# Optimization experiments

Measured on AMD Instinct MI355X. Metric: run time of the kernel, lower is better.

Reference implementation:

```python
import jax, jax.numpy as jnp
import numpy as np

LEVELS = ((64, 176), (32, 88), (16, 44), (8, 22))
S_TOTAL = sum(h * w for h, w in LEVELS)  # 14960
C = 128; HH = 8; HD = 16; R = 4; L = 4; P = 8
G = 32; PC_MIN = -4.0; PC_MAX = 4.0
NUM_CLASSES = 17; PROP = 3 + 3 + 4 + 1 + NUM_CLASSES  # 28


def _ln(x, g, b):
    m = x.mean(-1, keepdims=True)
    v = ((x - m) ** 2).mean(-1, keepdims=True)
    return (x - m) * jax.lax.rsqrt(v + 1e-5) * g + b


def setup_inputs() -> dict:
    key = jax.random.key(0)
    ks = jax.random.split(key, 20)
    B, N, CAM = 1, 1024, 6
    d = {}
    d['query'] = jax.random.normal(ks[0], (B, N, C), jnp.float32)
    d['gaussian_props'] = jax.random.normal(ks[1], (B, N, PROP), jnp.float32)
    d['ms_feats'] = jax.random.normal(ks[2], (B, CAM, S_TOTAL, C), jnp.float32)
    d['depth_maps'] = jax.random.uniform(ks[3], (B, CAM, 64, 176), jnp.float32, 0.5, 50.0)
    d['lidar2img'] = jax.random.normal(ks[4], (B, CAM, 4, 4), jnp.float32)
    d['img_h'] = 256
    d['img_w'] = 704
    w = lambda k, shp: jax.random.normal(k, shp, jnp.float32) * 0.02
    d['W_sc'] = w(ks[5], (3, 3, 3, C, C)); d['b_sc'] = jnp.zeros((C,), jnp.float32)
    d['sc_g'] = jnp.ones((C,), jnp.float32); d['sc_b'] = jnp.zeros((C,), jnp.float32)
    d['ref_off_w'] = w(ks[6], (C, R * 3)); d['ref_off_b'] = jnp.zeros((R * 3,), jnp.float32)
    d['off_w'] = w(ks[7], (C, HH * R * L * P * 2)); d['off_b'] = jnp.zeros((HH * R * L * P * 2,), jnp.float32)
    d['aw_w'] = w(ks[8], (C, HH * R * L * P)); d['aw_b'] = jnp.zeros((HH * R * L * P,), jnp.float32)
    d['val_w'] = w(ks[9], (C, C)); d['val_b'] = jnp.zeros((C,), jnp.float32)
    d['out_w'] = w(ks[10], (C, C)); d['out_b'] = jnp.zeros((C,), jnp.float32)
    d['an_g'] = jnp.ones((C,), jnp.float32); d['an_b'] = jnp.zeros((C,), jnp.float32)
    d['f1_w'] = w(ks[11], (C, 4 * C)); d['f1_b'] = jnp.zeros((4 * C,), jnp.float32)
    d['f2_w'] = w(ks[12], (4 * C, C)); d['f2_b'] = jnp.zeros((C,), jnp.float32)
    d['fn_g'] = jnp.ones((C,), jnp.float32); d['fn_b'] = jnp.zeros((C,), jnp.float32)
    d['p1_w'] = w(ks[13], (C, C)); d['p1_b'] = jnp.zeros((C,), jnp.float32)
    d['p2_w'] = w(ks[14], (C, PROP)); d['p2_b'] = jnp.zeros((PROP,), jnp.float32)
    return d


def _forward(query, gaussian_props, ms_feats, depth_maps, lidar2img,
             W_sc, b_sc, sc_g, sc_b, ref_off_w, ref_off_b, off_w, off_b,
             aw_w, aw_b, val_w, val_b, out_w, out_b, an_g, an_b,
             f1_w, f1_b, f2_w, f2_b, fn_g, fn_b, p1_w, p1_b, p2_w, p2_b,
             img_h, img_w):
    B, N, _ = query.shape
    CAM = ms_feats.shape[1]
    means = gaussian_props[..., :3]
    # ---- SparseConv3DBlock: scatter-mean voxelization, 3x3x3 conv, gather back ----
    vs = (PC_MAX - PC_MIN) / G
    vox = jnp.clip(jnp.floor((means - PC_MIN) / vs).astype(jnp.int32), 0, G - 1)
    flat = (vox[..., 0] * G + vox[..., 1]) * G + vox[..., 2]  # [B,N]
    bi = jnp.arange(B)[:, None]
    grid = jnp.zeros((B, G * G * G, C), query.dtype).at[bi, flat].add(query)
    cnt = jnp.zeros((B, G * G * G, 1), query.dtype).at[bi, flat].add(1.0)
    grid = (grid / jnp.maximum(cnt, 1.0)).reshape(B, G, G, G, C)
    grid = jax.lax.conv_general_dilated(grid, W_sc, (1, 1, 1), 'SAME',
                                        dimension_numbers=('NDHWC', 'DHWIO', 'NDHWC')) + b_sc
    grid = jax.nn.gelu(grid).reshape(B, G * G * G, C)
    query = _ln(query + grid[bi, flat], sc_g, sc_b)
    # ---- DeformableAttention3D ----
    fW = jnp.asarray(img_w, query.dtype); fH = jnp.asarray(img_h, query.dtype)
    ref3d = means[:, :, None, :] + (query @ ref_off_w + ref_off_b).reshape(B, N, R, 3)
    pts = jnp.concatenate([ref3d, jnp.ones_like(ref3d[..., :1])], -1)
    proj = jnp.einsum('bcij,bnrj->bcnri', lidar2img, pts)  # [B,CAM,N,R,4]
    z = proj[..., 2]; zc = jnp.maximum(z, 1e-5)
    u = proj[..., 0] / zc; v = proj[..., 1] / zc
    valid = (z > 1e-5) & (u >= 0) & (u < fW) & (v >= 0) & (v < fH)
    Hd, Wd = depth_maps.shape[2], depth_maps.shape[3]
    iu = jnp.clip((u / fW * Wd).astype(jnp.int32), 0, Wd - 1)
    iv = jnp.clip((v / fH * Hd).astype(jnp.int32), 0, Hd - 1)
    ds = jnp.take_along_axis(depth_maps.reshape(B, CAM, Hd * Wd),
                             (iv * Wd + iu).reshape(B, CAM, N * R), axis=2).reshape(B, CAM, N, R)
    wmask = jnp.exp(-jnp.abs(z - ds)) * valid.astype(query.dtype)  # [B,CAM,N,R]
    ref2 = jnp.stack([u / fW, v / fH], -1)  # [B,CAM,N,R,2]
    offs = (query @ off_w + off_b).reshape(B, N, HH, R, L, P, 2)
    attn = jax.nn.softmax((query @ aw_w + aw_b).reshape(B, N, HH, R * L * P), -1)
    attn = attn.reshape(B, N, HH, R, L, P)
    value = (ms_feats @ val_w + val_b).reshape(B, CAM, S_TOTAL, HH, HD)
    out = jnp.zeros((B, N, HH, HD), query.dtype)
    s0 = 0
    for l, (Hl, Wl) in enumerate(LEVELS):
        sz = Hl * Wl
        vl = value[:, :, s0:s0 + sz].transpose(0, 1, 3, 2, 4).reshape(B * CAM, HH, sz, HD)
        s0 += sz
        off_l = offs[:, :, :, :, l]  # [B,N,HH,R,P,2]
        loc = ref2[:, :, :, None, :, None, :] + off_l[:, None] / jnp.array([Wl, Hl], query.dtype)
        # loc: [B,CAM,N,HH,R,P,2] in normalized coords
        x = (loc[..., 0] * Wl - 0.5).transpose(0, 1, 3, 2, 4, 5).reshape(B * CAM, HH, N * R * P)
        y = (loc[..., 1] * Hl - 0.5).transpose(0, 1, 3, 2, 4, 5).reshape(B * CAM, HH, N * R * P)
        x0 = jnp.floor(x); y0 = jnp.floor(y); wx = x - x0; wy = y - y0
        x0i = jnp.clip(x0.astype(jnp.int32), 0, Wl - 1)
        x1i = jnp.clip(x0.astype(jnp.int32) + 1, 0, Wl - 1)
        y0i = jnp.clip(y0.astype(jnp.int32), 0, Hl - 1)
        y1i = jnp.clip(y0.astype(jnp.int32) + 1, 0, Hl - 1)
        g = lambda ix, iy: jnp.take_along_axis(vl, (iy * Wl + ix)[..., None], axis=2)
        samp = (((1 - wx) * (1 - wy))[..., None] * g(x0i, y0i)
                + (wx * (1 - wy))[..., None] * g(x1i, y0i)
                + ((1 - wx) * wy)[..., None] * g(x0i, y1i)
                + (wx * wy)[..., None] * g(x1i, y1i))  # [B*CAM,HH,N*R*P,HD]
        samp = samp.reshape(B, CAM, HH, N, R, P, HD)
        ws = attn[:, :, :, :, l, :][:, None].transpose(0, 1, 3, 2, 4, 5) * wmask[:, :, None, :, :, None]
        out = out + jnp.einsum('bchnrp,bchnrpd->bnhd', ws, samp)
    attn_out = out.reshape(B, N, C) @ out_w + out_b
    query = _ln(query + attn_out, an_g, an_b)
    query = _ln(query + (jax.nn.gelu(query @ f1_w + f1_b) @ f2_w + f2_b), fn_g, fn_b)
    props = gaussian_props + (jax.nn.gelu(query @ p1_w + p1_b) @ p2_w + p2_b)
    return query, props


def reference(query, gaussian_props, ms_feats, depth_maps, lidar2img,
              W_sc, b_sc, sc_g, sc_b, ref_off_w, ref_off_b, off_w, off_b,
              aw_w, aw_b, val_w, val_b, out_w, out_b, an_g, an_b,
              f1_w, f1_b, f2_w, f2_b, fn_g, fn_b, p1_w, p1_b, p2_w, p2_b,
              img_h, img_w):
    return _forward(query, gaussian_props, ms_feats, depth_maps, lidar2img,
                    W_sc, b_sc, sc_g, sc_b, ref_off_w, ref_off_b, off_w, off_b,
                    aw_w, aw_b, val_w, val_b, out_w, out_b, an_g, an_b,
                    f1_w, f1_b, f2_w, f2_b, fn_g, fn_b, p1_w, p1_b, p2_w, p2_b,
                    img_h, img_w)
```

## Files before the change

### kernel.cpp

```cpp
#include <hip/hip_runtime.h>
#include <hip/hip_bf16.h>
#include <math.h>

#define NQ    1024
#define CC    128
#define CAM   6
#define RR    4
#define LL    4
#define PP    8
#define HHD   8
#define HDD   16
#define GG    32
#define S_TOT 14960
#define PROPN 28
#define NTAP  27
#define MVAL  (CAM * S_TOT)
#define NVB   ((MVAL + 63) / 64)
#define NCVB  (8 * NTAP)

typedef __attribute__((ext_vector_type(8))) short bf16x8;
typedef __attribute__((ext_vector_type(4))) float f32x4;

__device__ __forceinline__ float gelu_tanh(float x) {
    return 0.5f * x * (1.0f + tanhf(0.7978845608028654f * (x + 0.044715f * x * x * x)));
}

__device__ __forceinline__ unsigned short f2bf(float f) {
    union { float f; unsigned int u; } x; x.f = f;
    unsigned int r = (x.u + 0x7FFFu + ((x.u >> 16) & 1u)) >> 16;
    return (unsigned short)r;
}

__device__ __forceinline__ float bf2f(short s) {
    union { unsigned int u; float f; } x;
    x.u = ((unsigned int)(unsigned short)s) << 16;
    return x.f;
}

__global__ void k_wt_scatter(const float* __restrict__ Wsc, unsigned short* __restrict__ WscT,
                             const float* __restrict__ valw, unsigned short* __restrict__ valwT,
                             const float* __restrict__ outw, unsigned short* __restrict__ outwT,
                             const float* __restrict__ p1w, unsigned short* __restrict__ p1wT,
                             const float* __restrict__ f1w, unsigned short* __restrict__ f1wT,
                             const float* __restrict__ f2w, unsigned short* __restrict__ f2wT,
                             const float* __restrict__ offw, unsigned short* __restrict__ offwT,
                             const float* __restrict__ aww, unsigned short* __restrict__ awwT,
                             const float* __restrict__ p2w, unsigned short* __restrict__ p2wT,
                             const float* __restrict__ p2b, float* __restrict__ p2bp,
                             const float* __restrict__ qin, const float* __restrict__ gp,
                             float* __restrict__ grid, float* __restrict__ cnt,
                             int* __restrict__ flatidx) {
    __shared__ float t[64][65];
    __shared__ int sflat[2];
    int z = blockIdx.z;
    int tid = threadIdx.x;

    if (z >= 63) {
        int half = tid >> 7, c = tid & 127;
        int n = ((z - 63) * 4 + (blockIdx.x * 2 + blockIdx.y)) * 2 + half;
        if (c == 0) {
            float mx = gp[n * PROPN + 0], my = gp[n * PROPN + 1], mz = gp[n * PROPN + 2];
            int vx = (int)floorf((mx + 4.0f) * 4.0f);
            int vy = (int)floorf((my + 4.0f) * 4.0f);
            int vz = (int)floorf((mz + 4.0f) * 4.0f);
            vx = min(max(vx, 0), GG - 1);
            vy = min(max(vy, 0), GG - 1);
            vz = min(max(vz, 0), GG - 1);
            int f = (vx * GG + vy) * GG + vz;
            sflat[half] = f;
            flatidx[n] = f;
            atomicAdd(&cnt[f], 1.0f);
        }
        __syncthreads();
        atomicAdd(&grid[(size_t)sflat[half] * CC + c], qin[(size_t)n * CC + c]);
        return;
    }

    int n0 = blockIdx.x * 64, k0 = blockIdx.y * 64;
    if (z == 62) {
#pragma unroll
        for (int it = 0; it < 16; ++it) {
            int idx = tid + it * 256;
            int r = idx >> 6, c = idx & 63;
            t[r][c] = (n0 + c < PROPN) ? p2w[(size_t)(k0 + r) * PROPN + n0 + c] : 0.f;
        }
        __syncthreads();
#pragma unroll
        for (int it = 0; it < 16; ++it) {
            int idx = tid + it * 256;
            int r = idx >> 6, c = idx & 63;
            p2wT[(size_t)(n0 + r) * 128 + k0 + c] = f2bf(t[c][r]);
        }
        if (blockIdx.x == 0 && blockIdx.y == 0 && tid < 128)
            p2bp[tid] = (tid < PROPN) ? p2b[tid] : 0.f;
        return;
    }
    const float* src; unsigned short* dst; int ss, ds;
    if (z < 27)       { src = Wsc + (size_t)z * 16384; dst = WscT + (size_t)z * 16384; ss = 128; ds = 128; }
    else if (z == 27) { src = valw; dst = valwT; ss = 128; ds = 128; }
    else if (z == 28) { src = outw; dst = outwT; ss = 128; ds = 128; }
    else if (z == 29) { src = p1w;  dst = p1wT;  ss = 128; ds = 128; }
    else if (z < 34)  { int q = z - 30; src = f1w + q * 128; dst = f1wT + (size_t)q * 16384; ss = 512;  ds = 128; }
    else if (z < 38)  { int q = z - 34; src = f2w + (size_t)q * 16384; dst = f2wT + q * 128; ss = 128;  ds = 512; }
    else if (z < 54)  { int q = z - 38; src = offw + q * 128; dst = offwT + (size_t)q * 16384; ss = 2048; ds = 128; }
    else              { int q = z - 54; src = aww + q * 128;  dst = awwT + (size_t)q * 16384; ss = 1024; ds = 128; }
#pragma unroll
    for (int it = 0; it < 16; ++it) {
        int idx = tid + it * 256;
        int r = idx >> 6, c = idx & 63;
        t[r][c] = src[(size_t)(k0 + r) * ss + n0 + c];
    }
    __syncthreads();
#pragma unroll
    for (int it = 0; it < 16; ++it) {
        int idx = tid + it * 256;
        int r = idx >> 6, c = idx & 63;
        dst[(size_t)(n0 + r) * ds + k0 + c] = f2bf(t[c][r]);
    }
}

union CVSm {
    struct { bf16x8 As[128 * 16]; bf16x8 Bs[128 * 16]; } c;
    struct { bf16x8 Bs[128 * 16]; unsigned short Os[64 * 128]; float sbias[128]; } v;
};
__global__ __launch_bounds__(256) void k_conv_val(
    const float* __restrict__ grid, const float* __restrict__ cnt,
    const int* __restrict__ flatidx, const unsigned short* __restrict__ WT,
    float* __restrict__ convacc27,
    const float* __restrict__ ms, const unsigned short* __restrict__ valwT,
    const float* __restrict__ valb, unsigned short* __restrict__ value)
{
    __shared__ CVSm sm;
    __shared__ int   nbase[128];
    __shared__ float nscale[128];
    int bx = blockIdx.x, tid = threadIdx.x;
    int lane = tid & 63, wv = tid >> 6;
    int r = lane & 15, q = lane >> 4;

    if (bx >= NCVB) {
        int vb = bx - NCVB;
        int m0 = vb * 64;
#pragma unroll
        for (int it = 0; it < 8; ++it) {
            int idx = tid + it * 256;
            int n = idx >> 4, c = idx & 15;
            sm.v.Bs[n * 16 + (c ^ (n & 15))] = *(const bf16x8*)(valwT + (size_t)n * 128 + c * 8);
        }
        if (tid < 128) sm.v.sbias[tid] = valb[tid];
        __syncthreads();

        int row = m0 + wv * 16 + r;
        int mg = min(row, MVAL - 1);
        const float* pA = ms + (size_t)mg * 128;

        f32x4 acc[8];
#pragma unroll
        for (int j = 0; j < 8; ++j)
#pragma unroll
            for (int e = 0; e < 4; ++e) acc[j][e] = 0.f;

#pragma unroll
        for (int ks = 0; ks < 4; ++ks) {
            const float* p = pA + ks * 32 + q * 8;
            float4 aa = *(const float4*)p;
            float4 bb = *(const float4*)(p + 4);
            bf16x8 af;
            af[0] = (short)f2bf(aa.x); af[1] = (short)f2bf(aa.y);
            af[2] = (short)f2bf(aa.z); af[3] = (short)f2bf(aa.w);
            af[4] = (short)f2bf(bb.x); af[5] = (short)f2bf(bb.y);
            af[6] = (short)f2bf(bb.z); af[7] = (short)f2bf(bb.w);
            bf16x8 bfr[8];
#pragma unroll
            for (int j = 0; j < 8; ++j)
                bfr[j] = sm.v.Bs[(j * 16 + r) * 16 + ((ks * 4 + q) ^ r)];
#pragma unroll
            for (int j = 0; j < 8; ++j)
                acc[j] = __builtin_amdgcn_mfma_f32_16x16x32_bf16(af, bfr[j], acc[j], 0, 0, 0);
        }

#pragma unroll
        for (int j = 0; j < 8; ++j)
#pragma unroll
            for (int e = 0; e < 4; ++e) {
                int rl = wv * 16 + q * 4 + e;
                sm.v.Os[rl * 128 + j * 16 + r] = f2bf(acc[j][e] + sm.v.sbias[j * 16 + r]);
            }
        __syncthreads();
#pragma unroll
        for (int it = 0; it < 2; ++it) {
            int idx = tid + it * 256;
            int rl = idx & 63, h = idx >> 6;
            int m = m0 + rl;
            if (m < MVAL) {
                int cam = m / S_TOT;
                int s = m - cam * S_TOT;
                int pos, HW, sb;
                if (s < 11264)      { pos = s;          HW = 11264; sb = 0; }
                else if (s < 14080) { pos = s - 11264;  HW = 2816;  sb = 11264; }
                else if (s < 14784) { pos = s - 14080;  HW = 704;   sb = 14080; }
                else                { pos = s - 14784;  HW = 176;   sb = 14784; }
                size_t dst = ((size_t)cam * S_TOT + sb) * CC
                           + (size_t)h * (HW * HDD) + (size_t)pos * HDD;
                *(bf16x8*)(value + dst)     = *(const bf16x8*)&sm.v.Os[rl * 128 + h * 16];
                *(bf16x8*)(value + dst + 8) = *(const bf16x8*)&sm.v.Os[rl * 128 + h * 16 + 8];
            }
        }
        return;
    }

    int tap = bx >> 3;
    int q0 = (bx & 7) * 128;
    int dz = tap / 9 - 1, dy = (tap / 3) % 3 - 1, dx = tap % 3 - 1;

    if (tid < 128) {
        int f = flatidx[q0 + tid];
        int nx = (f >> 10) + dz, ny = ((f >> 5) & 31) + dy, nz = (f & 31) + dx;
        bool ok = (nx >= 0 && nx < GG && ny >= 0 && ny < GG && nz >= 0 && nz < GG);
        int nf = ok ? (nx * GG + ny) * GG + nz : 0;
        nbase[tid] = nf;
        nscale[tid] = ok ? 1.0f / fmaxf(cnt[nf], 1.0f) : 0.f;
    }
    __syncthreads();
#pragma unroll
    for (int it = 0; it < 8; ++it) {
        int idx = tid + it * 256;
        int m = idx >> 4, c = idx & 15;
        const float* p = grid + (size_t)nbase[m] * CC + c * 8;
        float s = nscale[m];
        float4 a = *(const float4*)p;
        float4 b = *(const float4*)(p + 4);
        bf16x8 u;
        u[0] = (short)f2bf(a.x * s); u[1] = (short)f2bf(a.y * s);
        u[2] = (short)f2bf(a.z * s); u[3] = (short)f2bf(a.w * s);
        u[4] = (short)f2bf(b.x * s); u[5] = (short)f2bf(b.y * s);
        u[6] = (short)f2bf(b.z * s); u[7] = (short)f2bf(b.w * s);
        sm.c.As[m * 16 + (c ^ (m & 15))] = u;
    }
    const unsigned short* Wt = WT + (size_t)tap * CC * CC;
#pragma unroll
    for (int it = 0; it < 8; ++it) {
        int idx = tid + it * 256;
        int n = idx >> 4, c = idx & 15;
        bf16x8 w = *(const bf16x8*)(Wt + (size_t)n * CC + c * 8);
        sm.c.Bs[n * 16 + (c ^ (n & 15))] = w;
    }
    __syncthreads();

    int wr = (wv >> 1) * 64, wc = (wv & 1) * 64;
    f32x4 acc[4][4];
#pragma unroll
    for (int i = 0; i < 4; ++i)
#pragma unroll
        for (int j = 0; j < 4; ++j)
#pragma unroll
            for (int e = 0; e < 4; ++e) acc[i][j][e] = 0.f;
#pragma unroll
    for (int ks = 0; ks < 4; ++ks) {
        bf16x8 bfr[4];
#pragma unroll
        for (int j = 0; j < 4; ++j)
            bfr[j] = sm.c.Bs[(wc + j * 16 + r) * 16 + ((ks * 4 + q) ^ r)];
#pragma unroll
        for (int i = 0; i < 4; ++i) {
            bf16x8 af = sm.c.As[(wr + i * 16 + r) * 16 + ((ks * 4 + q) ^ r)];
#pragma unroll
            for (int j = 0; j < 4; ++j)
                acc[i][j] = __builtin_amdgcn_mfma_f32_16x16x32_bf16(af, bfr[j], acc[i][j], 0, 0, 0);
        }
    }
    float* dst = convacc27 + (size_t)tap * NQ * CC;
#pragma unroll
    for (int i = 0; i < 4; ++i)
#pragma unroll
        for (int e = 0; e < 4; ++e) {
            int m = q0 + wr + i * 16 + q * 4 + e;
#pragma unroll
            for (int j = 0; j < 4; ++j) {
                int col = wc + j * 16 + r;
                dst[(size_t)m * CC + col] = acc[i][j][e];
            }
        }
}

__global__ void k_ln_conv_proj(const float* __restrict__ a, const float* __restrict__ convacc27,
                               const float* __restrict__ bconv,
                               const float* __restrict__ g, const float* __restrict__ be,
                               float* __restrict__ out, unsigned short* __restrict__ outbf,
                               const float* __restrict__ refw, const float* __restrict__ refb,
                               const float* __restrict__ gp, const float* __restrict__ l2i,
                               const float* __restrict__ depth,
                               const int* __restrict__ ih, const int* __restrict__ iw,
                               float* __restrict__ wm, float* __restrict__ r2u,
                               float* __restrict__ r2v) {
    int n = blockIdx.x, c = threadIdx.x;
    float apart = 0.f;
#pragma unroll
    for (int t = 0; t < NTAP; ++t) apart += convacc27[((size_t)t * NQ + n) * CC + c];
    float x = a[n * CC + c] + gelu_tanh(apart + bconv[c]);
    __shared__ float w4[4];
    __shared__ float qrow[CC];
    __shared__ float ro[12];
    float s = x;
#pragma unroll
    for (int d = 1; d < 64; d <<= 1) s += __shfl_xor(s, d);
    if ((c & 63) == 0) w4[c >> 6] = s;
    __syncthreads();
    float m = (w4[0] + w4[1]) * (1.0f / CC);
    float dd = x - m;
    float v = dd * dd;
#pragma unroll
    for (int d = 1; d < 64; d <<= 1) v += __shfl_xor(v, d);
    if ((c & 63) == 0) w4[2 + (c >> 6)] = v;
    __syncthreads();
    float var = (w4[2] + w4[3]) * (1.0f / CC);
    float qv = dd * rsqrtf(var + 1e-5f) * g[c] + be[c];
    out[n * CC + c] = qv;
    outbf[n * CC + c] = f2bf(qv);
    qrow[c] = qv;
    __syncthreads();
    if (c < 12) {
        float sacc = refb[c];
#pragma unroll 4
        for (int k = 0; k < 128; ++k) sacc += qrow[k] * refw[k * 12 + c];
        ro[c] = sacc;
    }
    __syncthreads();
    if (c < 24) {
        int cam = c >> 2, r = c & 3;
        float fH = (float)(*ih), fW = (float)(*iw);
        const float* M = l2i + cam * 16;
        float px = gp[n * PROPN + 0] + ro[r * 3 + 0];
        float py = gp[n * PROPN + 1] + ro[r * 3 + 1];
        float pz = gp[n * PROPN + 2] + ro[r * 3 + 2];
        float p0 = M[0] * px + M[1] * py + M[2]  * pz + M[3];
        float p1 = M[4] * px + M[5] * py + M[6]  * pz + M[7];
        float p2 = M[8] * px + M[9] * py + M[10] * pz + M[11];
        float zc = fmaxf(p2, 1e-5f);
        float u = p0 / zc, vv = p1 / zc;
        bool valid = (p2 > 1e-5f) && (u >= 0.f) && (u < fW) && (vv >= 0.f) && (vv < fH);
        int iu = min(max((int)(u / fW * 176.f), 0), 175);
        int iv = min(max((int)(vv / fH * 64.f), 0), 63);
        float ds = depth[cam * 64 * 176 + iv * 176 + iu];
        int o = cam * (NQ * RR) + n * RR + r;
        wm[o]  = valid ? expf(-fabsf(p2 - ds)) : 0.f;
        r2u[o] = u / fW;
        r2v[o] = vv / fH;
    }
}

__global__ __launch_bounds__(256) void k_qhead(
    const unsigned short* __restrict__ Abf,
    const unsigned short* __restrict__ offwT, const float* __restrict__ offb,
    unsigned short* __restrict__ offsb,
    const unsigned short* __restrict__ awwT, const float* __restrict__ awb,
    unsigned short* __restrict__ attn)
{
    __shared__ bf16x8 Bs[128 * 16];
    int bx = blockIdx.x, tid = threadIdx.x;
    int lane = tid & 63, wv = tid >> 6;
    int r = lane & 15, q = lane >> 4;
    bool isoff = bx < 16;
    int n0 = (isoff ? bx : (bx - 16)) * 128;
    const unsigned short* WT = isoff ? offwT : awwT;
    int m0 = blockIdx.y * 128;
    int mw = m0 + wv * 32;

#pragma unroll
    for (int it = 0; it < 8; ++it) {
        int idx = tid + it * 256;
        int n = idx >> 4, c = idx & 15;
        Bs[n * 16 + (c ^ (n & 15))] = *(const bf16x8*)(WT + (size_t)(n0 + n) * 128 + c * 8);
    }
    __syncthreads();

    f32x4 acc[2][8];
#pragma unroll
    for (int i = 0; i < 2; ++i)
#pragma unroll
        for (int j = 0; j < 8; ++j)
#pragma unroll
            for (int e = 0; e < 4; ++e) acc[i][j][e] = 0.f;

#pragma unroll
    for (int ks = 0; ks < 4; ++ks) {
        bf16x8 af[2];
#pragma unroll
        for (int i = 0; i < 2; ++i)
            af[i] = *(const bf16x8*)(Abf + (size_t)(mw + i * 16 + r) * 128 + (ks * 4 + q) * 8);
#pragma unroll
        for (int j = 0; j < 8; ++j) {
            bf16x8 b = Bs[(j * 16 + r) * 16 + ((ks * 4 + q) ^ r)];
#pragma unroll
            for (int i = 0; i < 2; ++i)
                acc[i][j] = __builtin_amdgcn_mfma_f32_16x16x32_bf16(af[i], b, acc[i][j], 0, 0, 0);
        }
    }

    float bia[8];
    const float* bsrc = isoff ? offb : awb;
#pragma unroll
    for (int j = 0; j < 8; ++j) bia[j] = bsrc[n0 + j * 16 + r];

    if (isoff) {
#pragma unroll
        for (int i = 0; i < 2; ++i)
#pragma unroll
            for (int e = 0; e < 4; ++e) {
                int m = mw + i * 16 + q * 4 + e;
                unsigned short* orow = offsb + (size_t)m * 2048 + n0;
#pragma unroll
                for (int j = 0; j < 8; ++j)
                    orow[j * 16 + r] = f2bf(acc[i][j][e] + bia[j]);
            }
    } else {
#pragma unroll
        for (int i = 0; i < 2; ++i)
#pragma unroll
            for (int e = 0; e < 4; ++e) {
                float mx = -1e30f;
#pragma unroll
                for (int j = 0; j < 8; ++j) mx = fmaxf(mx, acc[i][j][e] + bia[j]);
#pragma unroll
                for (int d = 1; d < 16; d <<= 1) mx = fmaxf(mx, __shfl_xor(mx, d));
                float ex[8];
                float sum = 0.f;
#pragma unroll
                for (int j = 0; j < 8; ++j) { ex[j] = expf(acc[i][j][e] + bia[j] - mx); sum += ex[j]; }
#pragma unroll
                for (int d = 1; d < 16; d <<= 1) sum += __shfl_xor(sum, d);
                float inv = 1.0f / sum;
                int m = mw + i * 16 + q * 4 + e;
                unsigned short* orow = attn + (size_t)m * 1024 + n0;
#pragma unroll
                for (int j = 0; j < 8; ++j)
                    orow[j * 16 + r] = f2bf(ex[j] * inv);
            }
    }
}

__global__ __launch_bounds__(512) void k_sample(
                         const unsigned short* __restrict__ value,
                         const unsigned short* __restrict__ offsb,
                         const unsigned short* __restrict__ attn,
                         const float* __restrict__ wm,
                         const float* __restrict__ r2u, const float* __restrict__ r2v,
                         float* __restrict__ sampout) {
    const int Wl_[4] = {176, 88, 44, 22};
    const int Hl_[4] = {64, 32, 16, 8};
    const int s0_[4] = {0, 11264, 14080, 14784};
    int n = blockIdx.x, tid = threadIdx.x;
    __shared__ float s_attn[1024];
    __shared__ float s_offs[2048];
    __shared__ float s_wm[24], s_ru[24], s_rv[24];
    __shared__ float part[HHD][HDD];

    if (tid < 128) {
        bf16x8 v = *(const bf16x8*)(attn + (size_t)n * 1024 + tid * 8);
#pragma unroll
        for (int d = 0; d < 8; ++d) s_attn[tid * 8 + d] = bf2f(v[d]);
    }
    if (tid < 256) {
        bf16x8 v = *(const bf16x8*)(offsb + (size_t)n * 2048 + tid * 8);
#pragma unroll
        for (int d = 0; d < 8; ++d) s_offs[tid * 8 + d] = bf2f(v[d]);
    }
    if (tid < 24) {
        int cam = tid >> 2, r = tid & 3;
        int o = cam * (NQ * RR) + n * RR + r;
        s_wm[tid] = wm[o]; s_ru[tid] = r2u[o]; s_rv[tid] = r2v[o];
    }
    __syncthreads();

    int half = tid >> 8;
    int t8 = tid & 255;
    int h = t8 >> 5, slot = t8 & 31;
    int l = slot >> 3, p = slot & 7;
    int Wl = Wl_[l], Hl = Hl_[l];
    float fWl = (float)Wl, fHl = (float)Hl;
    size_t planeC = (size_t)s0_[l] * CC + (size_t)h * (Hl * Wl * HDD);
    float acc[16];
#pragma unroll
    for (int d = 0; d < 16; ++d) acc[d] = 0.f;

    for (int cr = half * 12; cr < half * 12 + 12; ++cr) {
        int cam = cr >> 2, r = cr & 3;
        float ws = s_attn[h * 128 + r * 32 + l * 8 + p] * s_wm[cr];
        if (ws == 0.f) continue;
        float ox = s_offs[h * 256 + r * 64 + l * 16 + p * 2 + 0];
        float oy = s_offs[h * 256 + r * 64 + l * 16 + p * 2 + 1];
        float x = s_ru[cr] * fWl + ox - 0.5f;
        float y = s_rv[cr] * fHl + oy - 0.5f;
        float xf = floorf(x), yf = floorf(y);
        float wx = x - xf, wy = y - yf;
        int x0 = min(max((int)xf, 0), Wl - 1);
        int x1 = min(max((int)xf + 1, 0), Wl - 1);
        int y0 = min(max((int)yf, 0), Hl - 1);
        int y1 = min(max((int)yf + 1, 0), Hl - 1);
        const unsigned short* base = value + (size_t)cam * S_TOT * CC + planeC;
        const unsigned short* p00 = base + (size_t)(y0 * Wl + x0) * HDD;
        const unsigned short* p01 = base + (size_t)(y0 * Wl + x1) * HDD;
        const unsigned short* p10 = base + (size_t)(y1 * Wl + x0) * HDD;
        const unsigned short* p11 = base + (size_t)(y1 * Wl + x1) * HDD;
        float w00 = ws * (1.f - wx) * (1.f - wy);
        float w01 = ws * wx * (1.f - wy);
        float w10 = ws * (1.f - wx) * wy;
        float w11 = ws * wx * wy;
        bf16x8 va0 = *(const bf16x8*)p00, va1 = *(const bf16x8*)(p00 + 8);
        bf16x8 vb0 = *(const bf16x8*)p01, vb1 = *(const bf16x8*)(p01 + 8);
        bf16x8 vc0 = *(const bf16x8*)p10, vc1 = *(const bf16x8*)(p10 + 8);
        bf16x8 vd0 = *(const bf16x8*)p11, vd1 = *(const bf16x8*)(p11 + 8);
#pragma unroll
        for (int d = 0; d < 8; ++d)
            acc[d] += w00 * bf2f(va0[d]) + w01 * bf2f(vb0[d]) + w10 * bf2f(vc0[d]) + w11 * bf2f(vd0[d]);
#pragma unroll
        for (int d = 0; d < 8; ++d)
            acc[8 + d] += w00 * bf2f(va1[d]) + w01 * bf2f(vb1[d]) + w10 * bf2f(vc1[d]) + w11 * bf2f(vd1[d]);
    }

#pragma unroll
    for (int d = 0; d < 16; ++d) {
        float a = acc[d];
#pragma unroll
        for (int s = 16; s >= 1; s >>= 1) a += __shfl_xor(a, s, 32);
        acc[d] = a;
    }
    if (half == 1 && slot == 0) {
#pragma unroll
        for (int d = 0; d < 16; ++d) part[h][d] = acc[d];
    }
    __syncthreads();
    if (half == 0 && slot == 0) {
#pragma unroll
        for (int d = 0; d < 16; ++d)
            sampout[(size_t)n * CC + h * HDD + d] = acc[d] + part[h][d];
    }
}

__global__ __launch_bounds__(512) void k_tail(
    const float* __restrict__ sampout,
    const unsigned short* __restrict__ outwT, const float* __restrict__ outb,
    const float* __restrict__ q1, const float* __restrict__ ang, const float* __restrict__ anb,
    const unsigned short* __restrict__ f1wT, const float* __restrict__ f1b,
    const unsigned short* __restrict__ f2wT, const float* __restrict__ f2b,
    const float* __restrict__ fng, const float* __restrict__ fnb,
    const unsigned short* __restrict__ p1wT, const float* __restrict__ p1b,
    const unsigned short* __restrict__ p2wT, const float* __restrict__ p2bp,
    const float* __restrict__ gp, float* __restrict__ outq, float* __restrict__ outp)
{
    __shared__ bf16x8 As[16 * 16];
    __shared__ bf16x8 Aff[16 * 64];
    __shared__ float xrow[16 * 128];
    __shared__ float q2s[16 * 128];
    unsigned short* Affu = (unsigned short*)Aff;
    unsigned short* As2u = (unsigned short*)Aff;
    int tid = threadIdx.x, m0 = blockIdx.x * 16;
    int lane = tid & 63, wv = tid >> 6;
    int wc = wv * 16;
    int r = lane & 15, q = lane >> 4;
    int lrow = tid >> 5, ls = tid & 31;

    bf16x8 b1[4];
#pragma unroll
    for (int ks = 0; ks < 4; ++ks)
        b1[ks] = *(const bf16x8*)(outwT + (size_t)(wc + r) * 128 + (ks * 4 + q) * 8);

    if (tid < 256) {
        int m = tid >> 4, c = tid & 15;
        const float* p = sampout + (size_t)(m0 + m) * 128 + c * 8;
        float4 a = *(const float4*)p;
        float4 b = *(const float4*)(p + 4);
        bf16x8 u;
        u[0] = (short)f2bf(a.x); u[1] = (short)f2bf(a.y);
        u[2] = (short)f2bf(a.z); u[3] = (short)f2bf(a.w);
        u[4] = (short)f2bf(b.x); u[5] = (short)f2bf(b.y);
        u[6] = (short)f2bf(b.z); u[7] = (short)f2bf(b.w);
        As[m * 16 + (c ^ m)] = u;
    }
    __syncthreads();

    f32x4 acc;
    bf16x8 a4[4];
#pragma unroll
    for (int ks = 0; ks < 4; ++ks) a4[ks] = As[r * 16 + ((ks * 4 + q) ^ r)];
#pragma unroll
    for (int e = 0; e < 4; ++e) acc[e] = 0.f;
#pragma unroll
    for (int ks = 0; ks < 4; ++ks)
        acc = __builtin_amdgcn_mfma_f32_16x16x32_bf16(a4[ks], b1[ks], acc, 0, 0, 0);
#pragma unroll
    for (int e = 0; e < 4; ++e) {
        int ml = q * 4 + e;
        int cl = wc + r;
        xrow[ml * 128 + cl] = acc[e] + outb[cl] + q1[(size_t)(m0 + ml) * 128 + cl];
    }
    __syncthreads();

    {
        float* xr = xrow + lrow * 128;
        float sum = 0.f;
#pragma unroll
        for (int e = ls; e < 128; e += 32) sum += xr[e];
#pragma unroll
        for (int d = 16; d; d >>= 1) sum += __shfl_xor(sum, d, 32);
        float mean = sum * (1.0f / 128.0f);
        float var = 0.f;
#pragma unroll
        for (int e = ls; e < 128; e += 32) { float dd = xr[e] - mean; var += dd * dd; }
#pragma unroll
        for (int d = 16; d; d >>= 1) var += __shfl_xor(var, d, 32);
        float rstd = rsqrtf(var * (1.0f / 128.0f) + 1e-5f);
#pragma unroll
        for (int e = ls; e < 128; e += 32)
            q2s[lrow * 128 + e] = (xr[e] - mean) * rstd * ang[e] + anb[e];
    }
    __syncthreads();
    if (tid < 256) {
        int m = tid >> 4, c = tid & 15;
        const float* p = q2s + m * 128 + c * 8;
        bf16x8 u;
#pragma unroll
        for (int d = 0; d < 8; ++d) u[d] = (short)f2bf(p[d]);
        As[m * 16 + (c ^ m)] = u;
    }
    __syncthreads();

#pragma unroll
    for (int ks = 0; ks < 4; ++ks) a4[ks] = As[r * 16 + ((ks * 4 + q) ^ r)];
    bf16x8 bcur[4];
#pragma unroll
    for (int ks = 0; ks < 4; ++ks)
        bcur[ks] = *(const bf16x8*)(f1wT + (size_t)(wc + r) * 128 + (ks * 4 + q) * 8);
#pragma unroll
    for (int nt = 0; nt < 4; ++nt) {
        bf16x8 bnx[4];
        if (nt < 3) {
#pragma unroll
            for (int ks = 0; ks < 4; ++ks)
                bnx[ks] = *(const bf16x8*)(f1wT + (size_t)(nt + 1) * 16384
                                            + (size_t)(wc + r) * 128 + (ks * 4 + q) * 8);
        }
#pragma unroll
        for (int e = 0; e < 4; ++e) acc[e] = 0.f;
#pragma unroll
        for (int ks = 0; ks < 4; ++ks)
            acc = __builtin_amdgcn_mfma_f32_16x16x32_bf16(a4[ks], bcur[ks], acc, 0, 0, 0);
#pragma unroll
        for (int e = 0; e < 4; ++e) {
            int ml = q * 4 + e;
            int col = nt * 128 + wc + r;
            float v = gelu_tanh(acc[e] + f1b[col]);
            Affu[(ml * 64 + ((col >> 3) ^ ml)) * 8 + (col & 7)] = f2bf(v);
        }
        if (nt < 3) {
#pragma unroll
            for (int ks = 0; ks < 4; ++ks) bcur[ks] = bnx[ks];
        }
    }
    __syncthreads();

#pragma unroll
    for (int e = 0; e < 4; ++e) acc[e] = 0.f;
#pragma unroll
    for (int ks = 0; ks < 4; ++ks)
        bcur[ks] = *(const bf16x8*)(f2wT + (size_t)(wc + r) * 512 + (ks * 4 + q) * 8);
#pragma unroll
    for (int kc = 0; kc < 4; ++kc) {
        bf16x8 bnx[4];
        if (kc < 3) {
#pragma unroll
            for (int ks = 0; ks < 4; ++ks)
                bnx[ks] = *(const bf16x8*)(f2wT + (size_t)(wc + r) * 512
                                            + ((kc + 1) * 16 + ks * 4 + q) * 8);
        }
#pragma unroll
        for (int ks = 0; ks < 4; ++ks) {
            bf16x8 af = Aff[r * 64 + ((kc * 16 + ks * 4 + q) ^ r)];
            acc = __builtin_amdgcn_mfma_f32_16x16x32_bf16(af, bcur[ks], acc, 0, 0, 0);
        }
        if (kc < 3) {
#pragma unroll
            for (int ks = 0; ks < 4; ++ks) bcur[ks] = bnx[ks];
        }
    }
#pragma unroll
    for (int e = 0; e < 4; ++e) {
        int ml = q * 4 + e;
        int cl = wc + r;
        xrow[ml * 128 + cl] = acc[e] + f2b[cl] + q2s[ml * 128 + cl];
    }
    __syncthreads();

    {
        float* xr = xrow + lrow * 128;
        float sum = 0.f;
#pragma unroll
        for (int e = ls; e < 128; e += 32) sum += xr[e];
#pragma unroll
        for (int d = 16; d; d >>= 1) sum += __shfl_xor(sum, d, 32);
        float mean = sum * (1.0f / 128.0f);
        float var = 0.f;
#pragma unroll
        for (int e = ls; e < 128; e += 32) { float dd = xr[e] - mean; var += dd * dd; }
#pragma unroll
        for (int d = 16; d; d >>= 1) var += __shfl_xor(var, d, 32);
        float rstd = rsqrtf(var * (1.0f / 128.0f) + 1e-5f);
        float* oq = outq + (size_t)(m0 + lrow) * 128;
#pragma unroll
        for (int e = ls; e < 128; e += 32) {
            float v = (xr[e] - mean) * rstd * fng[e] + fnb[e];
            oq[e] = v;
            q2s[lrow * 128 + e] = v;
        }
    }
    __syncthreads();
    if (tid < 256) {
        int m = tid >> 4, c = tid & 15;
        const float* p = q2s + m * 128 + c * 8;
        bf16x8 u;
#pragma unroll
        for (int d = 0; d < 8; ++d) u[d] = (short)f2bf(p[d]);
        As[m * 16 + (c ^ m)] = u;
    }
    __syncthreads();

#pragma unroll
    for (int ks = 0; ks < 4; ++ks) a4[ks] = As[r * 16 + ((ks * 4 + q) ^ r)];
#pragma unroll
    for (int ks = 0; ks < 4; ++ks)
        bcur[ks] = *(const bf16x8*)(p1wT + (size_t)(wc + r) * 128 + (ks * 4 + q) * 8);
#pragma unroll
    for (int ks = 0; ks < 4; ++ks)
        b1[ks] = *(const bf16x8*)(p2wT + (size_t)(wc + r) * 128 + (ks * 4 + q) * 8);
#pragma unroll
    for (int e = 0; e < 4; ++e) acc[e] = 0.f;
#pragma unroll
    for (int ks = 0; ks < 4; ++ks)
        acc = __builtin_amdgcn_mfma_f32_16x16x32_bf16(a4[ks], bcur[ks], acc, 0, 0, 0);
#pragma unroll
    for (int e = 0; e < 4; ++e) {
        int ml = q * 4 + e;
        int cl = wc + r;
        float v = gelu_tanh(acc[e] + p1b[cl]);
        As2u[(ml * 16 + ((cl >> 3) ^ ml)) * 8 + (cl & 7)] = f2bf(v);
    }
    __syncthreads();

#pragma unroll
    for (int e = 0; e < 4; ++e) acc[e] = 0.f;
#pragma unroll
    for (int ks = 0; ks < 4; ++ks) {
        bf16x8 af = Aff[r * 16 + ((ks * 4 + q) ^ r)];
        acc = __builtin_amdgcn_mfma_f32_16x16x32_bf16(af, b1[ks], acc, 0, 0, 0);
    }
#pragma unroll
    for (int e = 0; e < 4; ++e) {
        int m = m0 + q * 4 + e;
        int cl = wc + r;
        if (cl < PROPN)
            outp[(size_t)m * PROPN + cl] = acc[e] + p2bp[cl] + gp[(size_t)m * PROPN + cl];
    }
}

extern "C" void kernel_launch(void* const* d_in, const int* in_sizes, int n_in,
                              void* d_out, int out_size, void* d_ws, size_t ws_size,
                              hipStream_t stream) {
    const float* query = (const float*)d_in[0];
    const float* gp    = (const float*)d_in[1];
    const float* ms    = (const float*)d_in[2];
    const float* depth = (const float*)d_in[3];
    const float* l2i   = (const float*)d_in[4];
    const int*   ih    = (const int*)d_in[5];
    const int*   iw    = (const int*)d_in[6];
    const float* Wsc   = (const float*)d_in[7];
    const float* bsc   = (const float*)d_in[8];
    const float* scg   = (const float*)d_in[9];
    const float* scb   = (const float*)d_in[10];
    const float* refw  = (const float*)d_in[11];
    const float* refb  = (const float*)d_in[12];
    const float* offw  = (const float*)d_in[13];
    const float* offbi = (const float*)d_in[14];
    const float* aww   = (const float*)d_in[15];
    const float* awb   = (const float*)d_in[16];
    const float* valw  = (const float*)d_in[17];
    const float* valb  = (const float*)d_in[18];
    const float* outw  = (const float*)d_in[19];
    const float* outb  = (const float*)d_in[20];
    const float* ang   = (const float*)d_in[21];
    const float* anb   = (const float*)d_in[22];
    const float* f1w   = (const float*)d_in[23];
    const float* f1b   = (const float*)d_in[24];
    const float* f2w   = (const float*)d_in[25];
    const float* f2b   = (const float*)d_in[26];
    const float* fng   = (const float*)d_in[27];
    const float* fnb   = (const float*)d_in[28];
    const float* p1w   = (const float*)d_in[29];
    const float* p1b   = (const float*)d_in[30];
    const float* p2w   = (const float*)d_in[31];
    const float* p2b   = (const float*)d_in[32];

    float* outq = (float*)d_out;
    float* outp = outq + NQ * CC;

    float* ws = (float*)d_ws;
    size_t o = 0;
    float* grid    = ws + o; o += (size_t)GG * GG * GG * CC;
    float* cnt     = ws + o; o += GG * GG * GG;
    size_t zero_floats = o;
    int*   flatidx = (int*)(ws + o); o += NQ;
    float* convacc27 = ws + o; o += (size_t)NTAP * NQ * CC;
    float* q1      = ws + o; o += NQ * CC;
    float* wm      = ws + o; o += CAM * NQ * RR;
    float* r2u     = ws + o; o += CAM * NQ * RR;
    float* r2v     = ws + o; o += CAM * NQ * RR;
    float* sampout = ws + o; o += NQ * CC;
    float* p2bp    = ws + o; o += 128;
    unsigned short* u16base = (unsigned short*)(ws + o);
    size_t uo = 0;
    unsigned short* value = u16base + uo; uo += (size_t)CAM * S_TOT * CC;
    unsigned short* offsb = u16base + uo; uo += (size_t)NQ * 2048;
    unsigned short* attn  = u16base + uo; uo += (size_t)NQ * 1024;
    unsigned short* q1bf  = u16base + uo; uo += (size_t)NQ * CC;
    unsigned short* offwT = u16base + uo; uo += (size_t)2048 * 128;
    unsigned short* awwT  = u16base + uo; uo += (size_t)1024 * 128;
    unsigned short* valwT = u16base + uo; uo += 128 * 128;
    unsigned short* outwT = u16base + uo; uo += 128 * 128;
    unsigned short* f1wT  = u16base + uo; uo += 512 * 128;
    unsigned short* f2wT  = u16base + uo; uo += 128 * 512;
    unsigned short* p1wT  = u16base + uo; uo += 128 * 128;
    unsigned short* p2wT  = u16base + uo; uo += 128 * 128;
    unsigned short* WscT  = u16base + uo; uo += (size_t)27 * 128 * 128;
    (void)ws_size; (void)in_sizes; (void)n_in; (void)out_size;

    hipMemsetAsync(ws, 0, zero_floats * sizeof(float), stream);

    k_wt_scatter<<<dim3(2, 2, 63 + 128), 256, 0, stream>>>(
        Wsc, WscT, valw, valwT, outw, outwT, p1w, p1wT, f1w, f1wT, f2w, f2wT,
        offw, offwT, aww, awwT, p2w, p2wT, p2b, p2bp,
        query, gp, grid, cnt, flatidx);

    k_conv_val<<<dim3(NCVB + NVB), 256, 0, stream>>>(
        grid, cnt, flatidx, WscT, convacc27,
        ms, valwT, valb, value);

    k_ln_conv_proj<<<NQ, CC, 0, stream>>>(query, convacc27, bsc, scg, scb, q1, q1bf,
                                          refw, refb, gp, l2i, depth, ih, iw, wm, r2u, r2v);

    k_qhead<<<dim3(24, 8), 256, 0, stream>>>(q1bf, offwT, offbi, offsb, awwT, awb, attn);

    k_sample<<<NQ, 512, 0, stream>>>(value, offsb, attn, wm, r2u, r2v, sampout);

    k_tail<<<64, 512, 0, stream>>>(sampout, outwT, outb, q1, ang, anb,
                                   f1wT, f1b, f2wT, f2b, fng, fnb,
                                   p1wT, p1b, p2wT, p2bp, gp, outq, outp);
}
```

Measured before the change: 221.4 us.

## Shrink LDS in conv/value kernel, parallelize ref-offset dot, halve qhead tile

The value projection now writes bf16 outputs straight from registers with bias held in registers, dropping the LDS staging buffer and a barrier. The conv path loads the gathered grid rows straight from global memory into MFMA A fragments instead of staging them in LDS, which cuts shared memory per block. The 12-output reference-offset dot product is split across 96 threads with shuffle reductions. The qhead kernel processes 64 rows per block across twice as many blocks. These changes aim to raise occupancy and parallelism, at the cost of uncoalesced scattered 2-byte global stores and redundant global reads of grid rows.

```diff
diff --git a/kernel.cpp b/kernel.cpp
--- a/kernel.cpp
+++ b/kernel.cpp
@@ -119,10 +119,6 @@
     }
 }
 
-union CVSm {
-    struct { bf16x8 As[128 * 16]; bf16x8 Bs[128 * 16]; } c;
-    struct { bf16x8 Bs[128 * 16]; unsigned short Os[64 * 128]; float sbias[128]; } v;
-};
 __global__ __launch_bounds__(256) void k_conv_val(
     const float* __restrict__ grid, const float* __restrict__ cnt,
     const int* __restrict__ flatidx, const unsigned short* __restrict__ WT,
@@ -130,7 +126,7 @@
     const float* __restrict__ ms, const unsigned short* __restrict__ valwT,
     const float* __restrict__ valb, unsigned short* __restrict__ value)
 {
-    __shared__ CVSm sm;
+    __shared__ bf16x8 Bs[128 * 16];
     __shared__ int   nbase[128];
     __shared__ float nscale[128];
     int bx = blockIdx.x, tid = threadIdx.x;
@@ -144,14 +140,16 @@
         for (int it = 0; it < 8; ++it) {
             int idx = tid + it * 256;
             int n = idx >> 4, c = idx & 15;
-            sm.v.Bs[n * 16 + (c ^ (n & 15))] = *(const bf16x8*)(valwT + (size_t)n * 128 + c * 8);
-        }
-        if (tid < 128) sm.v.sbias[tid] = valb[tid];
+            Bs[n * 16 + (c ^ (n & 15))] = *(const bf16x8*)(valwT + (size_t)n * 128 + c * 8);
+        }
         __syncthreads();
 
         int row = m0 + wv * 16 + r;
         int mg = min(row, MVAL - 1);
         const float* pA = ms + (size_t)mg * 128;
+        float bia[8];
+#pragma unroll
+        for (int j = 0; j < 8; ++j) bia[j] = valb[j * 16 + r];
 
         f32x4 acc[8];
 #pragma unroll
@@ -172,25 +170,15 @@
             bf16x8 bfr[8];
 #pragma unroll
             for (int j = 0; j < 8; ++j)
-                bfr[j] = sm.v.Bs[(j * 16 + r) * 16 + ((ks * 4 + q) ^ r)];
+                bfr[j] = Bs[(j * 16 + r) * 16 + ((ks * 4 + q) ^ r)];
 #pragma unroll
             for (int j = 0; j < 8; ++j)
                 acc[j] = __builtin_amdgcn_mfma_f32_16x16x32_bf16(af, bfr[j], acc[j], 0, 0, 0);
         }
 
 #pragma unroll
-        for (int j = 0; j < 8; ++j)
-#pragma unroll
-            for (int e = 0; e < 4; ++e) {
-                int rl = wv * 16 + q * 4 + e;
-                sm.v.Os[rl * 128 + j * 16 + r] = f2bf(acc[j][e] + sm.v.sbias[j * 16 + r]);
-            }
-        __syncthreads();
-#pragma unroll
-        for (int it = 0; it < 2; ++it) {
-            int idx = tid + it * 256;
-            int rl = idx & 63, h = idx >> 6;
-            int m = m0 + rl;
+        for (int e = 0; e < 4; ++e) {
+            int m = m0 + wv * 16 + q * 4 + e;
             if (m < MVAL) {
                 int cam = m / S_TOT;
                 int s = m - cam * S_TOT;
@@ -199,10 +187,10 @@
                 else if (s < 14080) { pos = s - 11264;  HW = 2816;  sb = 11264; }
                 else if (s < 14784) { pos = s - 14080;  HW = 704;   sb = 14080; }
                 else                { pos = s - 14784;  HW = 176;   sb = 14784; }
-                size_t dst = ((size_t)cam * S_TOT + sb) * CC
-                           + (size_t)h * (HW * HDD) + (size_t)pos * HDD;
-                *(bf16x8*)(value + dst)     = *(const bf16x8*)&sm.v.Os[rl * 128 + h * 16];
-                *(bf16x8*)(value + dst + 8) = *(const bf16x8*)&sm.v.Os[rl * 128 + h * 16 + 8];
+                size_t base = ((size_t)cam * S_TOT + sb) * CC + (size_t)pos * HDD + r;
+#pragma unroll
+                for (int j = 0; j < 8; ++j)
+                    value[base + (size_t)j * (HW * HDD)] = f2bf(acc[j][e] + bia[j]);
             }
         }
         return;
@@ -220,29 +208,12 @@
         nbase[tid] = nf;
         nscale[tid] = ok ? 1.0f / fmaxf(cnt[nf], 1.0f) : 0.f;
     }
-    __syncthreads();
-#pragma unroll
-    for (int it = 0; it < 8; ++it) {
-        int idx = tid + it * 256;
-        int m = idx >> 4, c = idx & 15;
-        const float* p = grid + (size_t)nbase[m] * CC + c * 8;
-        float s = nscale[m];
-        float4 a = *(const float4*)p;
-        float4 b = *(const float4*)(p + 4);
-        bf16x8 u;
-        u[0] = (short)f2bf(a.x * s); u[1] = (short)f2bf(a.y * s);
-        u[2] = (short)f2bf(a.z * s); u[3] = (short)f2bf(a.w * s);
-        u[4] = (short)f2bf(b.x * s); u[5] = (short)f2bf(b.y * s);
-        u[6] = (short)f2bf(b.z * s); u[7] = (short)f2bf(b.w * s);
-        sm.c.As[m * 16 + (c ^ (m & 15))] = u;
-    }
     const unsigned short* Wt = WT + (size_t)tap * CC * CC;
 #pragma unroll
     for (int it = 0; it < 8; ++it) {
         int idx = tid + it * 256;
         int n = idx >> 4, c = idx & 15;
-        bf16x8 w = *(const bf16x8*)(Wt + (size_t)n * CC + c * 8);
-        sm.c.Bs[n * 16 + (c ^ (n & 15))] = w;
+        Bs[n * 16 + (c ^ (n & 15))] = *(const bf16x8*)(Wt + (size_t)n * CC + c * 8);
     }
     __syncthreads();
 
@@ -259,10 +230,19 @@
         bf16x8 bfr[4];
 #pragma unroll
         for (int j = 0; j < 4; ++j)
-            bfr[j] = sm.c.Bs[(wc + j * 16 + r) * 16 + ((ks * 4 + q) ^ r)];
+            bfr[j] = Bs[(wc + j * 16 + r) * 16 + ((ks * 4 + q) ^ r)];
 #pragma unroll
         for (int i = 0; i < 4; ++i) {
-            bf16x8 af = sm.c.As[(wr + i * 16 + r) * 16 + ((ks * 4 + q) ^ r)];
+            int row = wr + i * 16 + r;
+            const float* p = grid + (size_t)nbase[row] * CC + (ks * 4 + q) * 8;
+            float s = nscale[row];
+            float4 aa = *(const float4*)p;
+            float4 bb = *(const float4*)(p + 4);
+            bf16x8 af;
+            af[0] = (short)f2bf(aa.x * s); af[1] = (short)f2bf(aa.y * s);
+            af[2] = (short)f2bf(aa.z * s); af[3] = (short)f2bf(aa.w * s);
+            af[4] = (short)f2bf(bb.x * s); af[5] = (short)f2bf(bb.y * s);
+            af[6] = (short)f2bf(bb.z * s); af[7] = (short)f2bf(bb.w * s);
 #pragma unroll
             for (int j = 0; j < 4; ++j)
                 acc[i][j] = __builtin_amdgcn_mfma_f32_16x16x32_bf16(af, bfr[j], acc[i][j], 0, 0, 0);
@@ -292,14 +272,14 @@
                                const int* __restrict__ ih, const int* __restrict__ iw,
                                float* __restrict__ wm, float* __restrict__ r2u,
                                float* __restrict__ r2v) {
-    int n = blockIdx.x, c = threadIdx.x;
-    float apart = 0.f;
-#pragma unroll
-    for (int t = 0; t < NTAP; ++t) apart += convacc27[((size_t)t * NQ + n) * CC + c];
-    float x = a[n * CC + c] + gelu_tanh(apart + bconv[c]);
     __shared__ float w4[4];
     __shared__ float qrow[CC];
     __shared__ float ro[12];
+    int n = blockIdx.x, c = threadIdx.x;
+    float apart = 0.f;
+#pragma unroll
+    for (int t = 0; t < NTAP; ++t) apart += convacc27[((size_t)t * NQ + n) * CC + c];
+    float x = a[n * CC + c] + gelu_tanh(apart + bconv[c]);
     float s = x;
 #pragma unroll
     for (int d = 1; d < 64; d <<= 1) s += __shfl_xor(s, d);
@@ -318,11 +298,17 @@
     outbf[n * CC + c] = f2bf(qv);
     qrow[c] = qv;
     __syncthreads();
-    if (c < 12) {
-        float sacc = refb[c];
-#pragma unroll 4
-        for (int k = 0; k < 128; ++k) sacc += qrow[k] * refw[k * 12 + c];
-        ro[c] = sacc;
+    if (c < 96) {
+        int dg = c >> 3, ll = c & 7;
+        float sacc = 0.f;
+#pragma unroll
+        for (int k = 0; k < 16; ++k) {
+            int kk = ll * 16 + k;
+            sacc += qrow[kk] * refw[kk * 12 + dg];
+        }
+#pragma unroll
+        for (int d = 4; d; d >>= 1) sacc += __shfl_xor(sacc, d, 8);
+        if (ll == 0) ro[dg] = sacc + refb[dg];
     }
     __syncthreads();
     if (c < 24) {
@@ -362,8 +348,8 @@
     bool isoff = bx < 16;
     int n0 = (isoff ? bx : (bx - 16)) * 128;
     const unsigned short* WT = isoff ? offwT : awwT;
-    int m0 = blockIdx.y * 128;
-    int mw = m0 + wv * 32;
+    int m0 = blockIdx.y * 64;
+    int mw = m0 + wv * 16;
 
 #pragma unroll
     for (int it = 0; it < 8; ++it) {
@@ -373,26 +359,19 @@
     }
     __syncthreads();
 
-    f32x4 acc[2][8];
-#pragma unroll
-    for (int i = 0; i < 2; ++i)
-#pragma unroll
-        for (int j = 0; j < 8; ++j)
-#pragma unroll
-            for (int e = 0; e < 4; ++e) acc[i][j][e] = 0.f;
+    f32x4 acc[8];
+#pragma unroll
+    for (int j = 0; j < 8; ++j)
+#pragma unroll
+        for (int e = 0; e < 4; ++e) acc[j][e] = 0.f;
 
 #pragma unroll
     for (int ks = 0; ks < 4; ++ks) {
-        bf16x8 af[2];
-#pragma unroll
-        for (int i = 0; i < 2; ++i)
-            af[i] = *(const bf16x8*)(Abf + (size_t)(mw + i * 16 + r) * 128 + (ks * 4 + q) * 8);
+        bf16x8 af = *(const bf16x8*)(Abf + (size_t)(mw + r) * 128 + (ks * 4 + q) * 8);
 #pragma unroll
         for (int j = 0; j < 8; ++j) {
             bf16x8 b = Bs[(j * 16 + r) * 16 + ((ks * 4 + q) ^ r)];
-#pragma unroll
-            for (int i = 0; i < 2; ++i)
-                acc[i][j] = __builtin_amdgcn_mfma_f32_16x16x32_bf16(af[i], b, acc[i][j], 0, 0, 0);
+            acc[j] = __builtin_amdgcn_mfma_f32_16x16x32_bf16(af, b, acc[j], 0, 0, 0);
         }
     }
 
@@ -403,38 +382,34 @@
 
     if (isoff) {
 #pragma unroll
-        for (int i = 0; i < 2; ++i)
-#pragma unroll
-            for (int e = 0; e < 4; ++e) {
-                int m = mw + i * 16 + q * 4 + e;
-                unsigned short* orow = offsb + (size_t)m * 2048 + n0;
-#pragma unroll
-                for (int j = 0; j < 8; ++j)
-                    orow[j * 16 + r] = f2bf(acc[i][j][e] + bia[j]);
-            }
+        for (int e = 0; e < 4; ++e) {
+            int m = mw + q * 4 + e;
+            unsigned short* orow = offsb + (size_t)m * 2048 + n0;
+#pragma unroll
+            for (int j = 0; j < 8; ++j)
+                orow[j * 16 + r] = f2bf(acc[j][e] + bia[j]);
+        }
     } else {
 #pragma unroll
-        for (int i = 0; i < 2; ++i)
-#pragma unroll
-            for (int e = 0; e < 4; ++e) {
-                float mx = -1e30f;
-#pragma unroll
-                for (int j = 0; j < 8; ++j) mx = fmaxf(mx, acc[i][j][e] + bia[j]);
-#pragma unroll
-                for (int d = 1; d < 16; d <<= 1) mx = fmaxf(mx, __shfl_xor(mx, d));
-                float ex[8];
-                float sum = 0.f;
-#pragma unroll
-                for (int j = 0; j < 8; ++j) { ex[j] = expf(acc[i][j][e] + bia[j] - mx); sum += ex[j]; }
-#pragma unroll
-                for (int d = 1; d < 16; d <<= 1) sum += __shfl_xor(sum, d);
-                float inv = 1.0f / sum;
-                int m = mw + i * 16 + q * 4 + e;
-                unsigned short* orow = attn + (size_t)m * 1024 + n0;
-#pragma unroll
-                for (int j = 0; j < 8; ++j)
-                    orow[j * 16 + r] = f2bf(ex[j] * inv);
-            }
+        for (int e = 0; e < 4; ++e) {
+            float mx = -1e30f;
+#pragma unroll
+            for (int j = 0; j < 8; ++j) mx = fmaxf(mx, acc[j][e] + bia[j]);
+#pragma unroll
+            for (int d = 1; d < 16; d <<= 1) mx = fmaxf(mx, __shfl_xor(mx, d));
+            float ex[8];
+            float sum = 0.f;
+#pragma unroll
+            for (int j = 0; j < 8; ++j) { ex[j] = expf(acc[j][e] + bia[j] - mx); sum += ex[j]; }
+#pragma unroll
+            for (int d = 1; d < 16; d <<= 1) sum += __shfl_xor(sum, d);
+            float inv = 1.0f / sum;
+            int m = mw + q * 4 + e;
+            unsigned short* orow = attn + (size_t)m * 1024 + n0;
+#pragma unroll
+            for (int j = 0; j < 8; ++j)
+                orow[j * 16 + r] = f2bf(ex[j] * inv);
+        }
     }
 }
 
@@ -725,9 +700,10 @@
 
 #pragma unroll
     for (int ks = 0; ks < 4; ++ks) a4[ks] = As[r * 16 + ((ks * 4 + q) ^ r)];
+    bf16x8 bcur2[4];
 #pragma unroll
     for (int ks = 0; ks < 4; ++ks)
-        bcur[ks] = *(const bf16x8*)(p1wT + (size_t)(wc + r) * 128 + (ks * 4 + q) * 8);
+        bcur2[ks] = *(const bf16x8*)(p1wT + (size_t)(wc + r) * 128 + (ks * 4 + q) * 8);
 #pragma unroll
     for (int ks = 0; ks < 4; ++ks)
         b1[ks] = *(const bf16x8*)(p2wT + (size_t)(wc + r) * 128 + (ks * 4 + q) * 8);
@@ -735,7 +711,7 @@
     for (int e = 0; e < 4; ++e) acc[e] = 0.f;
 #pragma unroll
     for (int ks = 0; ks < 4; ++ks)
-        acc = __builtin_amdgcn_mfma_f32_16x16x32_bf16(a4[ks], bcur[ks], acc, 0, 0, 0);
+        acc = __builtin_amdgcn_mfma_f32_16x16x32_bf16(a4[ks], bcur2[ks], acc, 0, 0, 0);
 #pragma unroll
     for (int e = 0; e < 4; ++e) {
         int ml = q * 4 + e;
@@ -842,10 +818,11 @@
         grid, cnt, flatidx, WscT, convacc27,
         ms, valwT, valb, value);
 
-    k_ln_conv_proj<<<NQ, CC, 0, stream>>>(query, convacc27, bsc, scg, scb, q1, q1bf,
-                                          refw, refb, gp, l2i, depth, ih, iw, wm, r2u, r2v);
-
-    k_qhead<<<dim3(24, 8), 256, 0, stream>>>(q1bf, offwT, offbi, offsb, awwT, awb, attn);
+    k_ln_conv_proj<<<NQ, CC, 0, stream>>>(
+        query, convacc27, bsc, scg, scb, q1, q1bf,
+        refw, refb, gp, l2i, depth, ih, iw, wm, r2u, r2v);
+
+    k_qhead<<<dim3(24, 16), 256, 0, stream>>>(q1bf, offwT, offbi, offsb, awwT, awb, attn);
 
     k_sample<<<NQ, 512, 0, stream>>>(value, offsb, attn, wm, r2u, r2v, sampout);
 
```

After: 214.0 us (median of 2 runs). 1.03x faster.
